# Optimization experiments

Measured on AMD Instinct MI355X. Metric: run time of the kernel, lower is better.

## Reference

```python
import jax, jax.numpy as jnp
import numpy as np

B, T, DE, DD, A, FN, FS = 32, 2000, 512, 1024, 128, 32, 16
TEMPERATURE = 1.0


def setup_inputs() -> dict:
    key = jax.random.key(0)
    ks = jax.random.split(key, 10)
    input_enc = jax.random.normal(ks[0], (B, T, DE), dtype=jnp.float32)
    # lengths in [T//2, T] so no zero-length utterances
    enc_lengths = jax.random.randint(ks[1], (B,), T // 2, T + 1, dtype=jnp.int32)
    input_dec = jax.random.normal(ks[2], (B, DD), dtype=jnp.float32)
    # prev_att: previous-step attention weights (masked, normalized)
    prev_att = jax.random.uniform(ks[3], (B, T), dtype=jnp.float32)
    pad = jnp.arange(T)[None, :] >= enc_lengths[:, None]
    prev_att = jnp.where(pad, 0.0, prev_att)
    prev_att = prev_att / jnp.sum(prev_att, axis=1, keepdims=True)
    # parameters
    conv_w = jax.random.normal(ks[4], (FN, 1, 2 * FS + 1), dtype=jnp.float32) * 0.1  # [out,in,k]
    enc_w = jax.random.normal(ks[5], (A, DE), dtype=jnp.float32) * 0.04
    dec_w = jax.random.normal(ks[6], (A, DD), dtype=jnp.float32) * 0.03
    att_w = jax.random.normal(ks[7], (A, FN), dtype=jnp.float32) * 0.17
    att_b = jnp.zeros((A,), dtype=jnp.float32)
    out_w = jax.random.normal(ks[8], (1, A), dtype=jnp.float32) * 0.09
    return dict(input_enc=input_enc, enc_lengths=enc_lengths, input_dec=input_dec,
                prev_att=prev_att, conv_w=conv_w, enc_w=enc_w, dec_w=dec_w,
                att_w=att_w, att_b=att_b, out_w=out_w)


def reference(input_enc, enc_lengths, input_dec, prev_att,
              conv_w, enc_w, dec_w, att_w, att_b, out_w):
    b, t, _ = input_enc.shape
    fs = (conv_w.shape[-1] - 1) // 2  # 'same' padding
    # padding mask: True at padded positions t >= length
    mask = jnp.arange(t)[None, :] >= enc_lengths[:, None]  # [B,T]
    # location features: Conv1d over prev attention, 1 -> FN channels, same length
    conv = jax.lax.conv_general_dilated(
        prev_att[:, None, :], conv_w, window_strides=(1,),
        padding=[(fs, fs)], dimension_numbers=("NCH", "OIH", "NCH"))  # [B,FN,T]
    loc_feat = conv.transpose(0, 2, 1)  # [B,T,FN]
    projected_att = loc_feat @ att_w.T + att_b        # [B,T,A]
    projected_enc = input_enc @ enc_w.T               # [B,T,A]
    projected_dec = (input_dec @ dec_w.T)[:, None, :]  # [B,1,A]
    score = jnp.squeeze(jnp.tanh(projected_att + projected_enc + projected_dec) @ out_w.T, -1)  # [B,T]
    score = jnp.where(mask, -jnp.inf, score)
    att_weight = jax.nn.softmax(TEMPERATURE * score, axis=1)  # [B,T]
    context = jnp.einsum("btd,bt->bd", input_enc, att_weight)  # [B,DE]
    return context, att_weight
```

## Files before the change

### kernel.cpp

```cpp
#include <hip/hip_runtime.h>
#include <hip/hip_bf16.h>
#include <math.h>

#define B_ 32
#define T_ 2000
#define DE_ 512
#define DD_ 1024
#define A_ 128
#define FN_ 32
#define FS_ 16
#define KW_ (2*FS_+1)

typedef __bf16 bf16x8 __attribute__((ext_vector_type(8)));
typedef __bf16 bf16x4 __attribute__((ext_vector_type(4)));
typedef float f32x4 __attribute__((ext_vector_type(4)));

#define BT 64
#define LSTR 40

__device__ __forceinline__ void load_lds16(const void* g, void* l) {
    __builtin_amdgcn_global_load_lds(
        (const __attribute__((address_space(1))) unsigned int*)g,
        (__attribute__((address_space(3))) unsigned int*)l, 16, 0, 0);
}

__global__ __launch_bounds__(256) void prep_kernel(
    const float* __restrict__ enc_w, const float* __restrict__ att_w,
    const float* __restrict__ input_dec, const float* __restrict__ dec_w,
    const float* __restrict__ att_b,
    __bf16* __restrict__ enc_bf, __bf16* __restrict__ att_bf,
    float* __restrict__ pdec, float* __restrict__ ctx_un )
{
    int bx = blockIdx.x, tid = threadIdx.x;
    if (bx < 64) {
        int i = bx * 256 + tid;
        float4 v = ((const float4*)enc_w)[i];
        bf16x4 o;
        o[0] = (__bf16)v.x; o[1] = (__bf16)v.y; o[2] = (__bf16)v.z; o[3] = (__bf16)v.w;
        *(bf16x4*)(enc_bf + (size_t)i * 4) = o;
        if (i < (A_ * FN_) / 4) {
            float4 w = ((const float4*)att_w)[i];
            bf16x4 p;
            p[0] = (__bf16)w.x; p[1] = (__bf16)w.y; p[2] = (__bf16)w.z; p[3] = (__bf16)w.w;
            *(bf16x4*)(att_bf + (size_t)i * 4) = p;
        }
    } else if (bx < 192) {
        int pb = bx - 64;
        int b  = pb >> 2;
        int a0 = (pb & 3) * 32;
        int al = tid >> 3;
        int kg = tid & 7;
        int a  = a0 + al;
        const float4* w = (const float4*)(dec_w + (size_t)a * DD_);
        const float4* x = (const float4*)(input_dec + (size_t)b * DD_);
        float acc = 0.f;
        #pragma unroll 8
        for (int j = 0; j < 32; j++) {
            int i4 = kg + j * 8;
            float4 wv = w[i4], xv = x[i4];
            acc += wv.x * xv.x + wv.y * xv.y + wv.z * xv.z + wv.w * xv.w;
        }
        acc += __shfl_xor(acc, 1, 64);
        acc += __shfl_xor(acc, 2, 64);
        acc += __shfl_xor(acc, 4, 64);
        if (kg == 0) pdec[b * A_ + a] = acc + att_b[a];
    } else {
        int idx = (bx - 192) * 256 + tid;
        if (idx < (B_ * DE_ + B_) / 4 + 1)
            ((float4*)ctx_un)[idx] = make_float4(0.f, 0.f, 0.f, 0.f);
    }
}

__global__ __launch_bounds__(256, 4) void score_kernel(
    const float* __restrict__ input_enc, const __bf16* __restrict__ enc_bf,
    const float* __restrict__ prev_att,  const float* __restrict__ conv_w,
    const __bf16* __restrict__ att_bf,   const float* __restrict__ pdec,
    const float* __restrict__ out_w,     const int* __restrict__ lengths,
    float* __restrict__ wbuf, float* __restrict__ ctx_un,
    float* __restrict__ denom)
{
    __shared__ __align__(16) char Bt[16384];
    __shared__ float pa_s[BT + 2 * FS_];
    __shared__ float cw_s[KW_ * FN_];
    __shared__ __align__(16) __bf16 loc_s[BT * LSTR];
    __shared__ float w_s[BT];

    const int tid = threadIdx.x;
    const int b  = blockIdx.y;
    const int t0 = blockIdx.x * BT;
    const int len = lengths[b];

    for (int j = tid; j < BT + 2 * FS_; j += 256) {
        int t = t0 - FS_ + j;
        pa_s[j] = (t >= 0 && t < T_) ? prev_att[b * T_ + t] : 0.f;
    }
    for (int idx = tid; idx < FN_ * KW_; idx += 256) {
        int f = idx / KW_, k = idx % KW_;
        cw_s[k * FN_ + f] = conv_w[idx];
    }
    __syncthreads();

    {
        int f = tid & 31, r0 = tid >> 5;
        for (int r = r0; r < BT; r += 8) {
            float acc = 0.f;
            #pragma unroll
            for (int k = 0; k < KW_; k++) acc += pa_s[r + k] * cw_s[k * FN_ + f];
            loc_s[r * LSTR + f] = (__bf16)acc;
        }
    }
    __syncthreads();

    const int lane = tid & 63;
    const int wv   = tid >> 6;
    const int col  = lane & 15;
    const int grp  = lane >> 4;
    const int rowb = wv * 16 + col;
    const int t_row = t0 + rowb;
    const int t_clamp = t_row < T_ ? t_row : T_ - 1;
    const int sw = (col & 7);

    f32x4 acc[8];
    const f32x4 zero = (f32x4){0.f, 0.f, 0.f, 0.f};

    {
        bf16x8 afrag = *(const bf16x8*)(loc_s + rowb * LSTR + grp * 8);
        #pragma unroll
        for (int i = 0; i < 8; i++) {
            bf16x8 bfrag = *(const bf16x8*)(att_bf + (size_t)(i * 16 + col) * FN_ + grp * 8);
            acc[i] = __builtin_amdgcn_mfma_f32_16x16x32_bf16(afrag, bfrag, zero, 0, 0, 0);
        }
    }

    const float* arow = input_enc + ((size_t)(b * T_ + t_clamp)) * DE_ + grp * 8;

    for (int kc = 0; kc < DE_; kc += 64) {
        #pragma unroll
        for (int j = 0; j < 4; j++) {
            int s  = j * 256 + tid;
            int r  = s >> 3;
            int cp = s & 7;
            int c  = cp ^ (r & 7);
            load_lds16(enc_bf + (size_t)r * DE_ + kc + c * 8,
                       Bt + j * 4096 + wv * 1024);
        }
        float4 a00 = *(const float4*)(arow + kc);
        float4 a01 = *(const float4*)(arow + kc + 4);
        float4 a10 = *(const float4*)(arow + kc + 32);
        float4 a11 = *(const float4*)(arow + kc + 36);
        __syncthreads();

        bf16x8 af;
        af[0] = (__bf16)a00.x; af[1] = (__bf16)a00.y;
        af[2] = (__bf16)a00.z; af[3] = (__bf16)a00.w;
        af[4] = (__bf16)a01.x; af[5] = (__bf16)a01.y;
        af[6] = (__bf16)a01.z; af[7] = (__bf16)a01.w;
        #pragma unroll
        for (int i = 0; i < 8; i++) {
            bf16x8 bfrag = *(const bf16x8*)(Bt + (i * 16 + col) * 128 + ((grp ^ sw) * 16));
            acc[i] = __builtin_amdgcn_mfma_f32_16x16x32_bf16(af, bfrag, acc[i], 0, 0, 0);
        }
        af[0] = (__bf16)a10.x; af[1] = (__bf16)a10.y;
        af[2] = (__bf16)a10.z; af[3] = (__bf16)a10.w;
        af[4] = (__bf16)a11.x; af[5] = (__bf16)a11.y;
        af[6] = (__bf16)a11.z; af[7] = (__bf16)a11.w;
        #pragma unroll
        for (int i = 0; i < 8; i++) {
            bf16x8 bfrag = *(const bf16x8*)(Bt + (i * 16 + col) * 128 + (((4 + grp) ^ sw) * 16));
            acc[i] = __builtin_amdgcn_mfma_f32_16x16x32_bf16(af, bfrag, acc[i], 0, 0, 0);
        }
        __syncthreads();
    }

    float s[4] = {0.f, 0.f, 0.f, 0.f};
    float Mabs = 0.f;
    #pragma unroll
    for (int i = 0; i < 8; i++) {
        int a = i * 16 + col;
        float ow = out_w[a];
        Mabs += fabsf(ow);
        float bias = pdec[b * A_ + a];
        #pragma unroll
        for (int r = 0; r < 4; r++) {
            float v = acc[i][r] + bias;
            v = fminf(fmaxf(v, -15.f), 15.f);
            float e = __expf(2.f * v);
            s[r] += ow * ((e - 1.f) / (e + 1.f));
        }
    }
    #pragma unroll
    for (int r = 0; r < 4; r++) {
        s[r] += __shfl_xor(s[r], 1, 64);
        s[r] += __shfl_xor(s[r], 2, 64);
        s[r] += __shfl_xor(s[r], 4, 64);
        s[r] += __shfl_xor(s[r], 8, 64);
    }
    Mabs += __shfl_xor(Mabs, 1, 64);
    Mabs += __shfl_xor(Mabs, 2, 64);
    Mabs += __shfl_xor(Mabs, 4, 64);
    Mabs += __shfl_xor(Mabs, 8, 64);

    if (col == 0) {
        #pragma unroll
        for (int r = 0; r < 4; r++) {
            int rl = wv * 16 + grp * 4 + r;
            int t = t0 + rl;
            float w = 0.f;
            if (t < len) w = __expf(s[r] - Mabs);
            w_s[rl] = w;
            if (t < T_) wbuf[b * T_ + t] = w;
        }
    }
    __syncthreads();

    if (tid < 64) {
        float w = w_s[tid];
        w += __shfl_xor(w, 1, 64);
        w += __shfl_xor(w, 2, 64);
        w += __shfl_xor(w, 4, 64);
        w += __shfl_xor(w, 8, 64);
        w += __shfl_xor(w, 16, 64);
        w += __shfl_xor(w, 32, 64);
        if (tid == 0) atomicAdd(&denom[b], w);
    }

    int n_eff = len - t0;
    if (n_eff > BT) n_eff = BT;
    if (n_eff > 0) {
        int d0 = tid * 2;
        const float* ebase = input_enc + ((size_t)(b * T_ + t0)) * DE_ + d0;
        float cx = 0.f, cy = 0.f;
        #pragma unroll 8
        for (int t = 0; t < n_eff; t++) {
            float w = w_s[t];
            float2 v = *(const float2*)(ebase + (size_t)t * DE_);
            cx += w * v.x;
            cy += w * v.y;
        }
        atomicAdd(&ctx_un[b * DE_ + d0 + 0], cx);
        atomicAdd(&ctx_un[b * DE_ + d0 + 1], cy);
    }
}

__global__ __launch_bounds__(256) void finalize_kernel(
    const float* __restrict__ wbuf, const float* __restrict__ ctx_un,
    const float* __restrict__ denom, float* __restrict__ out)
{
    int bx = blockIdx.x, tid = threadIdx.x;
    if (bx < 64) {
        int i4 = bx * 256 + tid;
        if (i4 < (B_ * T_) / 4) {
            int b = i4 / (T_ / 4);
            float inv = 1.f / denom[b];
            float4 w = ((const float4*)wbuf)[i4];
            w.x *= inv; w.y *= inv; w.z *= inv; w.w *= inv;
            ((float4*)(out + B_ * DE_))[i4] = w;
        }
    } else {
        int j = (bx - 64) * 256 + tid;
        int b = j / (DE_ / 4);
        float inv = 1.f / denom[b];
        float4 c = ((const float4*)ctx_un)[j];
        c.x *= inv; c.y *= inv; c.z *= inv; c.w *= inv;
        ((float4*)out)[j] = c;
    }
}

extern "C" void kernel_launch(void* const* d_in, const int* in_sizes, int n_in,
                              void* d_out, int out_size, void* d_ws, size_t ws_size,
                              hipStream_t stream)
{
    const float* input_enc   = (const float*)d_in[0];
    const int*   enc_lengths = (const int*)d_in[1];
    const float* input_dec   = (const float*)d_in[2];
    const float* prev_att    = (const float*)d_in[3];
    const float* conv_w      = (const float*)d_in[4];
    const float* enc_w       = (const float*)d_in[5];
    const float* dec_w       = (const float*)d_in[6];
    const float* att_w       = (const float*)d_in[7];
    const float* att_b       = (const float*)d_in[8];
    const float* out_w       = (const float*)d_in[9];

    float* out = (float*)d_out;
    char* ws = (char*)d_ws;
    float*  pdec   = (float*)ws;
    float*  wbuf   = (float*)(ws + 16384);
    __bf16* enc_bf = (__bf16*)(ws + 272384);
    __bf16* att_bf = (__bf16*)(ws + 403456);
    float*  ctx_un = (float*)(ws + 411648);
    float*  denom  = (float*)(ws + 477184);

    prep_kernel<<<209, 256, 0, stream>>>(enc_w, att_w, input_dec, dec_w, att_b,
                                         enc_bf, att_bf, pdec, ctx_un);

    dim3 sgrid((T_ + BT - 1) / BT, B_);
    score_kernel<<<sgrid, 256, 0, stream>>>(input_enc, enc_bf, prev_att, conv_w,
                                            att_bf, pdec, out_w, enc_lengths,
                                            wbuf, ctx_un, denom);

    finalize_kernel<<<80, 256, 0, stream>>>(wbuf, ctx_un, denom, out);
}
```

Measured before the change: 225.9 us.

## Double-buffer enc weight tiles, skip fully padded blocks, vectorize context loop

Blocks whose tile starts past the utterance length now write zero weights and exit early, skipping the GEMM and context work on padding. The projection main loop moves to 32-wide K steps with a double-buffered LDS tile: the next slice's async LDS loads and the next activation row loads are issued before the current MFMAs, with a new XOR swizzle. The context accumulation uses float4 loads with two time-groups per block, and the weight stores become a single float4 write. This adds one barrier per K step and more live registers, which may reduce occupancy.

```diff
diff --git a/kernel.cpp b/kernel.cpp
--- a/kernel.cpp
+++ b/kernel.cpp
@@ -83,12 +83,38 @@
     __shared__ float pa_s[BT + 2 * FS_];
     __shared__ float cw_s[KW_ * FN_];
     __shared__ __align__(16) __bf16 loc_s[BT * LSTR];
-    __shared__ float w_s[BT];
+    __shared__ __align__(16) float w_s[BT];
 
     const int tid = threadIdx.x;
     const int b  = blockIdx.y;
     const int t0 = blockIdx.x * BT;
     const int len = lengths[b];
+
+    if (t0 >= len) {
+        int t = t0 + tid;
+        if (tid < BT && t < T_) wbuf[b * T_ + t] = 0.f;
+        return;
+    }
+
+    const int lane = tid & 63;
+    const int wv   = tid >> 6;
+    const int col  = lane & 15;
+    const int grp  = lane >> 4;
+    const int rowb = wv * 16 + col;
+    const int t_row = t0 + rowb;
+    const int t_clamp = t_row < T_ ? t_row : T_ - 1;
+    const float* arow = input_enc + ((size_t)(b * T_ + t_clamp)) * DE_ + grp * 8;
+
+    #pragma unroll
+    for (int j = 0; j < 2; j++) {
+        int s  = j * 256 + tid;
+        int r  = s >> 2;
+        int c  = (s & 3) ^ (r & 3);
+        load_lds16(enc_bf + (size_t)r * DE_ + c * 8,
+                   Bt + j * 4096 + wv * 1024);
+    }
+    float4 p0 = *(const float4*)(arow);
+    float4 p1 = *(const float4*)(arow + 4);
 
     for (int j = tid; j < BT + 2 * FS_; j += 256) {
         int t = t0 - FS_ + j;
@@ -111,15 +137,6 @@
     }
     __syncthreads();
 
-    const int lane = tid & 63;
-    const int wv   = tid >> 6;
-    const int col  = lane & 15;
-    const int grp  = lane >> 4;
-    const int rowb = wv * 16 + col;
-    const int t_row = t0 + rowb;
-    const int t_clamp = t_row < T_ ? t_row : T_ - 1;
-    const int sw = (col & 7);
-
     f32x4 acc[8];
     const f32x4 zero = (f32x4){0.f, 0.f, 0.f, 0.f};
 
@@ -132,44 +149,38 @@
         }
     }
 
-    const float* arow = input_enc + ((size_t)(b * T_ + t_clamp)) * DE_ + grp * 8;
-
-    for (int kc = 0; kc < DE_; kc += 64) {
-        #pragma unroll
-        for (int j = 0; j < 4; j++) {
-            int s  = j * 256 + tid;
-            int r  = s >> 3;
-            int cp = s & 7;
-            int c  = cp ^ (r & 7);
-            load_lds16(enc_bf + (size_t)r * DE_ + kc + c * 8,
-                       Bt + j * 4096 + wv * 1024);
-        }
-        float4 a00 = *(const float4*)(arow + kc);
-        float4 a01 = *(const float4*)(arow + kc + 4);
-        float4 a10 = *(const float4*)(arow + kc + 32);
-        float4 a11 = *(const float4*)(arow + kc + 36);
+    const int dsoff = (grp ^ (col & 3)) * 16;
+
+    #pragma unroll
+    for (int k = 0; k < 16; k++) {
         __syncthreads();
-
+        float4 n0, n1;
+        if (k < 15) {
+            int kc_next = (k + 1) * 32;
+            char* half = Bt + (((k + 1) & 1) << 13);
+            #pragma unroll
+            for (int j = 0; j < 2; j++) {
+                int s  = j * 256 + tid;
+                int r  = s >> 2;
+                int c  = (s & 3) ^ (r & 3);
+                load_lds16(enc_bf + (size_t)r * DE_ + kc_next + c * 8,
+                           half + j * 4096 + wv * 1024);
+            }
+            n0 = *(const float4*)(arow + kc_next);
+            n1 = *(const float4*)(arow + kc_next + 4);
+        }
         bf16x8 af;
-        af[0] = (__bf16)a00.x; af[1] = (__bf16)a00.y;
-        af[2] = (__bf16)a00.z; af[3] = (__bf16)a00.w;
-        af[4] = (__bf16)a01.x; af[5] = (__bf16)a01.y;
-        af[6] = (__bf16)a01.z; af[7] = (__bf16)a01.w;
+        af[0] = (__bf16)p0.x; af[1] = (__bf16)p0.y;
+        af[2] = (__bf16)p0.z; af[3] = (__bf16)p0.w;
+        af[4] = (__bf16)p1.x; af[5] = (__bf16)p1.y;
+        af[6] = (__bf16)p1.z; af[7] = (__bf16)p1.w;
+        const char* half = Bt + ((k & 1) << 13);
         #pragma unroll
         for (int i = 0; i < 8; i++) {
-            bf16x8 bfrag = *(const bf16x8*)(Bt + (i * 16 + col) * 128 + ((grp ^ sw) * 16));
+            bf16x8 bfrag = *(const bf16x8*)(half + (i * 16 + col) * 64 + dsoff);
             acc[i] = __builtin_amdgcn_mfma_f32_16x16x32_bf16(af, bfrag, acc[i], 0, 0, 0);
         }
-        af[0] = (__bf16)a10.x; af[1] = (__bf16)a10.y;
-        af[2] = (__bf16)a10.z; af[3] = (__bf16)a10.w;
-        af[4] = (__bf16)a11.x; af[5] = (__bf16)a11.y;
-        af[6] = (__bf16)a11.z; af[7] = (__bf16)a11.w;
-        #pragma unroll
-        for (int i = 0; i < 8; i++) {
-            bf16x8 bfrag = *(const bf16x8*)(Bt + (i * 16 + col) * 128 + (((4 + grp) ^ sw) * 16));
-            acc[i] = __builtin_amdgcn_mfma_f32_16x16x32_bf16(af, bfrag, acc[i], 0, 0, 0);
-        }
-        __syncthreads();
+        p0 = n0; p1 = n1;
     }
 
     float s[4] = {0.f, 0.f, 0.f, 0.f};
@@ -201,15 +212,16 @@
     Mabs += __shfl_xor(Mabs, 8, 64);
 
     if (col == 0) {
+        int tb = wv * 16 + grp * 4;
+        float4 wvec;
+        float* wp = &wvec.x;
         #pragma unroll
         for (int r = 0; r < 4; r++) {
-            int rl = wv * 16 + grp * 4 + r;
-            int t = t0 + rl;
-            float w = 0.f;
-            if (t < len) w = __expf(s[r] - Mabs);
-            w_s[rl] = w;
-            if (t < T_) wbuf[b * T_ + t] = w;
-        }
+            int t = t0 + tb + r;
+            wp[r] = (t < len) ? __expf(s[r] - Mabs) : 0.f;
+        }
+        *(float4*)(w_s + tb) = wvec;
+        if (t0 + tb < T_) *(float4*)(wbuf + b * T_ + t0 + tb) = wvec;
     }
     __syncthreads();
 
@@ -226,19 +238,21 @@
 
     int n_eff = len - t0;
     if (n_eff > BT) n_eff = BT;
-    if (n_eff > 0) {
-        int d0 = tid * 2;
+    {
+        int tg = tid >> 7;
+        int d0 = (tid & 127) * 4;
         const float* ebase = input_enc + ((size_t)(b * T_ + t0)) * DE_ + d0;
-        float cx = 0.f, cy = 0.f;
-        #pragma unroll 8
-        for (int t = 0; t < n_eff; t++) {
+        float cx = 0.f, cy = 0.f, cz = 0.f, cw = 0.f;
+        #pragma unroll 4
+        for (int t = tg; t < n_eff; t += 2) {
             float w = w_s[t];
-            float2 v = *(const float2*)(ebase + (size_t)t * DE_);
-            cx += w * v.x;
-            cy += w * v.y;
+            float4 v = *(const float4*)(ebase + (size_t)t * DE_);
+            cx += w * v.x; cy += w * v.y; cz += w * v.z; cw += w * v.w;
         }
         atomicAdd(&ctx_un[b * DE_ + d0 + 0], cx);
         atomicAdd(&ctx_un[b * DE_ + d0 + 1], cy);
+        atomicAdd(&ctx_un[b * DE_ + d0 + 2], cz);
+        atomicAdd(&ctx_un[b * DE_ + d0 + 3], cw);
     }
 }
 
```

New measurement: 228.0 us. Within noise of the previous version (+0.9%).
